# Kernel optimization log

Measured on AMD Instinct MI355X. Metric: run time of the kernel, lower is better.

Reference implementation:

```python
import jax, jax.numpy as jnp
import numpy as np

N = 100000
IN_CH, HID_CH, OUT_CH = 128, 128, 64
E = 1600000


def gcn_layer(x, W, b, src, dst, num_nodes):
    """PyG GCNConv: add self-loops, symmetric deg^-1/2 normalization,
    x' = D^-1/2 (A+I) D^-1/2 (x W) + b."""
    # degrees including self-loops (deg = 1 + in-degree with unit edge weights)
    ones = jnp.ones(dst.shape[0], dtype=x.dtype)
    deg = jnp.ones(num_nodes, dtype=x.dtype).at[dst].add(ones)
    dinv = jax.lax.rsqrt(deg)
    h = x @ W  # [N, out_dim] -- transform before propagate (PyG order)
    # neighbor messages
    norm = dinv[src] * dinv[dst]                      # [E]
    msg = h[src] * norm[:, None]                      # [E, out_dim] (traffic-bound)
    agg = jax.ops.segment_sum(msg, dst, num_segments=num_nodes)
    # self-loop contribution: norm_ii = dinv[i]^2
    agg = agg + h * (dinv * dinv)[:, None]
    return agg + b


def setup_inputs() -> dict:
    key = jax.random.key(0)
    ks = jax.random.split(key, 7)
    x = jax.random.normal(ks[0], (N, IN_CH), dtype=jnp.float32)
    edge_index = jax.random.randint(ks[1], (2, E), 0, N, dtype=jnp.int64)
    # Glorot-style init like PyG GCNConv
    W1 = jax.random.normal(ks[2], (IN_CH, HID_CH), dtype=jnp.float32) * (1.0 / np.sqrt(IN_CH))
    b1 = jnp.zeros((HID_CH,), dtype=jnp.float32)
    W2 = jax.random.normal(ks[3], (HID_CH, OUT_CH), dtype=jnp.float32) * (1.0 / np.sqrt(HID_CH))
    b2 = jnp.zeros((OUT_CH,), dtype=jnp.float32)
    return {"x": x, "edge_index": edge_index, "W1": W1, "b1": b1, "W2": W2, "b2": b2}


def reference(x, edge_index, W1, b1, W2, b2):
    src, dst = edge_index[0], edge_index[1]
    h = gcn_layer(x, W1, b1, src, dst, N)
    h = jax.nn.relu(h)  # dropout is identity in eval mode
    out = gcn_layer(h, W2, b2, src, dst, N)
    return out
```

## Files before the change

### kernel.cpp

```cpp
#include <hip/hip_runtime.h>
#include <hip/hip_fp16.h>

#define NNODES 100000
#define NEDGES 1600000
#define IN_C   128
#define HID_C  128
#define OUT_C  64

#define CAP     64
#define OVF_MAX 4096

#define BUCKET_SHIFT 7
#define BUCKET_NODES 128
#define NB ((NNODES + BUCKET_NODES - 1) / BUCKET_NODES)
#define BCAP 3072
#define BCNT_STRIDE 16
#define EB 4096
#define NBLK_A ((NEDGES + EB - 1) / EB)

typedef __attribute__((ext_vector_type(8))) _Float16 half8;
typedef __attribute__((ext_vector_type(4))) _Float16 half4;
typedef __attribute__((ext_vector_type(4))) float floatx4;

__device__ __forceinline__ long long load_idx(const void* p, long long i, int is64) {
  return is64 ? ((const long long*)p)[i] : (long long)((const int*)p)[i];
}

__global__ void detect_idx_kernel(const void* eidx, int* flag) {
  const unsigned* w = (const unsigned*)eidx;
  int lane = threadIdx.x & 63;
  unsigned v = w[2 * lane + 1];
  unsigned long long bad = __ballot(v != 0u);
  if (lane == 0) *flag = (bad == 0ull) ? 1 : 0;
}


__global__ void zero_misc_kernel(int* bcnt, int* ovf_cnt, int* ovfA_cnt) {
  int i = blockIdx.x * 256 + threadIdx.x;
  if (i < NB * BCNT_STRIDE) bcnt[i] = 0;
  if (i == 0) { *ovf_cnt = 0; *ovfA_cnt = 0; }
}

__global__ __launch_bounds__(256) void binA_kernel(const void* __restrict__ eidx,
                                                   const int* __restrict__ flag,
                                                   int* __restrict__ bcnt,
                                                   unsigned* __restrict__ buf,
                                                   int* __restrict__ ovfA_cnt,
                                                   int2* __restrict__ ovfA) {
  __shared__ unsigned se[EB];
  __shared__ unsigned short be[EB];
  __shared__ int hist[NB];
  __shared__ int base[NB];
  __shared__ int ofs[NB];
  const int tid = threadIdx.x;
  const int e0 = blockIdx.x * EB;
  const int e1 = min(e0 + EB, NEDGES);
  const int m = e1 - e0;
  const int is64 = *flag;

  for (int b = tid; b < NB; b += 256) { hist[b] = 0; ofs[b] = 0; }
  __syncthreads();

  for (int k = tid; k < m; k += 256) {
    int e = e0 + k;
    int s = (int)load_idx(eidx, e, is64);
    int d = (int)load_idx(eidx, (long long)NEDGES + e, is64);
    int b = d >> BUCKET_SHIFT;
    se[k] = (unsigned)s | ((unsigned)(d & (BUCKET_NODES - 1)) << 17);
    be[k] = (unsigned short)b;
    atomicAdd(&hist[b], 1);
  }
  __syncthreads();

  int rot = (blockIdx.x * 131) % NB;
  for (int idx = tid; idx < NB; idx += 256) {
    int b = idx + rot;
    if (b >= NB) b -= NB;
    int h = hist[b];
    if (h > 0) base[b] = atomicAdd(&bcnt[b * BCNT_STRIDE], h);
  }
  __syncthreads();

  for (int k = tid; k < m; k += 256) {
    unsigned u = se[k];
    int b = be[k];
    int ko = atomicAdd(&ofs[b], 1);
    int slot = base[b] + ko;
    if (slot < BCAP) {
      buf[(size_t)b * BCAP + slot] = u;
    } else {
      int p = atomicAdd(ovfA_cnt, 1);
      if (p < OVF_MAX)
        ovfA[p] = make_int2((int)(u & 0x1FFFFu),
                            (b << BUCKET_SHIFT) | (int)(u >> 17));
    }
  }
}

__global__ __launch_bounds__(256) void binB_kernel(const int* __restrict__ bcnt,
                                                   const unsigned* __restrict__ buf,
                                                   int* __restrict__ cnt,
                                                   float* __restrict__ dinv,
                                                   int* __restrict__ pad_csr,
                                                   int* __restrict__ ovf_cnt,
                                                   int2* __restrict__ ovf) {
  __shared__ int pad[BUCKET_NODES * CAP];
  __shared__ int lcnt[BUCKET_NODES];
  const int b = blockIdx.x;
  const int tid = threadIdx.x;
  const int node0 = b << BUCKET_SHIFT;

  if (tid < BUCKET_NODES) lcnt[tid] = 0;
  __syncthreads();

  const int n = min(bcnt[b * BCNT_STRIDE], BCAP);
  for (int k = tid; k < n; k += 256) {
    unsigned u = buf[(size_t)b * BCAP + k];
    int s = (int)(u & 0x1FFFFu);
    int dl = (int)(u >> 17);
    int slot = atomicAdd(&lcnt[dl], 1);
    if (slot < CAP) {
      pad[dl * CAP + slot] = s;
    } else {
      int p = atomicAdd(ovf_cnt, 1);
      if (p < OVF_MAX) ovf[p] = make_int2(s, node0 + dl);
    }
  }
  __syncthreads();

  constexpr int I4PN = CAP / 4;
  for (int q = tid; q < BUCKET_NODES * I4PN; q += 256) {
    int dl = q / I4PN;
    int gn = node0 + dl;
    if (gn < NNODES) {
      int c = (q % I4PN) * 4;
      *(int4*)&pad_csr[(size_t)gn * CAP + c] = *(const int4*)&pad[dl * CAP + c];
    }
  }
  if (tid < BUCKET_NODES && node0 + tid < NNODES) {
    int c = lcnt[tid];
    cnt[node0 + tid] = c;
    dinv[node0 + tid] = rsqrtf((float)(c + 1));
  }
}

__global__ void fixup_kernel(const int* __restrict__ ovfA_cnt,
                             const int2* __restrict__ ovfA,
                             int* __restrict__ cnt, float* __restrict__ dinv,
                             int* __restrict__ pad_csr,
                             int* __restrict__ ovf_cnt, int2* __restrict__ ovf) {
  int n = min(*ovfA_cnt, OVF_MAX);
  for (int t = threadIdx.x; t < n; t += 256) {
    int2 p = ovfA[t];
    int k = atomicAdd(&cnt[p.y], 1);
    if (k < CAP) {
      pad_csr[(size_t)p.y * CAP + k] = p.x;
    } else {
      int q = atomicAdd(ovf_cnt, 1);
      if (q < OVF_MAX) ovf[q] = p;
    }
  }
  __syncthreads();
  for (int t = threadIdx.x; t < n; t += 256) {
    int node = ovfA[t].y;
    dinv[node] = rsqrtf((float)(cnt[node] + 1));
  }
}

struct F8 {
  float x0, x1, x2, x3, x4, x5, x6, x7;
};

__device__ __forceinline__ void add_h8(F8& a, const __half* p) {
  int4 r = *(const int4*)p;
  const __half2* h = (const __half2*)&r;
  float2 f0 = __half22float2(h[0]);
  float2 f1 = __half22float2(h[1]);
  float2 f2 = __half22float2(h[2]);
  float2 f3 = __half22float2(h[3]);
  a.x0 += f0.x; a.x1 += f0.y; a.x2 += f1.x; a.x3 += f1.y;
  a.x4 += f2.x; a.x5 += f2.y; a.x6 += f3.x; a.x7 += f3.y;
}

template <int C, bool RELU, bool OUT16>
__global__ __launch_bounds__(256) void gather_kernel(const int* __restrict__ cnt,
                                                     const int* __restrict__ pad_csr,
                                                     const float* __restrict__ dinv,
                                                     const __half* __restrict__ Hs,
                                                     const float* __restrict__ bias,
                                                     const int* __restrict__ ovf_cnt,
                                                     const int2* __restrict__ ovf,
                                                     void* __restrict__ OutPtr) {
  constexpr int TPN = C / 16;
  int gid = blockIdx.x * 256 + threadIdx.x;
  int i = gid / TPN;
  int c16 = (gid % TPN) * 16;
  if (i >= NNODES) return;

  const float di = dinv[i];
  const int deg = cnt[i];
  const int beg = i * CAP;
  const int end = beg + min(deg, CAP);
  const int* __restrict__ lst = pad_csr;
  const __half* __restrict__ Hb = Hs + c16;

  F8 a0l = {}, a0h = {}, a1l = {}, a1h = {};
  {
    const __half* p = Hb + (size_t)i * C;
    add_h8(a0l, p);
    add_h8(a0h, p + 8);
  }

  int j = beg;
  for (; j + 8 <= end; j += 8) {
    int4 sa = *(const int4*)&lst[j];
    int4 sb = *(const int4*)&lst[j + 4];
    const __half* p0 = Hb + (size_t)sa.x * C;
    const __half* p1 = Hb + (size_t)sa.y * C;
    const __half* p2 = Hb + (size_t)sa.z * C;
    const __half* p3 = Hb + (size_t)sa.w * C;
    add_h8(a0l, p0); add_h8(a0h, p0 + 8);
    add_h8(a1l, p1); add_h8(a1h, p1 + 8);
    add_h8(a0l, p2); add_h8(a0h, p2 + 8);
    add_h8(a1l, p3); add_h8(a1h, p3 + 8);
    const __half* p4 = Hb + (size_t)sb.x * C;
    const __half* p5 = Hb + (size_t)sb.y * C;
    const __half* p6 = Hb + (size_t)sb.z * C;
    const __half* p7 = Hb + (size_t)sb.w * C;
    add_h8(a0l, p4); add_h8(a0h, p4 + 8);
    add_h8(a1l, p5); add_h8(a1h, p5 + 8);
    add_h8(a0l, p6); add_h8(a0h, p6 + 8);
    add_h8(a1l, p7); add_h8(a1h, p7 + 8);
  }
  for (; j + 2 <= end; j += 2) {
    const __half* p0 = Hb + (size_t)lst[j] * C;
    const __half* p1 = Hb + (size_t)lst[j + 1] * C;
    add_h8(a0l, p0); add_h8(a0h, p0 + 8);
    add_h8(a1l, p1); add_h8(a1h, p1 + 8);
  }
  if (j < end) {
    const __half* p0 = Hb + (size_t)lst[j] * C;
    add_h8(a0l, p0); add_h8(a0h, p0 + 8);
  }

  if (deg > CAP) {
    int n = min(*ovf_cnt, OVF_MAX);
    for (int t = 0; t < n; ++t) {
      int2 p = ovf[t];
      if (p.y == i) {
        const __half* q = Hb + (size_t)p.x * C;
        add_h8(a0l, q); add_h8(a0h, q + 8);
      }
    }
  }

  float s0 = a0l.x0 + a1l.x0, s1 = a0l.x1 + a1l.x1;
  float s2 = a0l.x2 + a1l.x2, s3 = a0l.x3 + a1l.x3;
  float s4 = a0l.x4 + a1l.x4, s5 = a0l.x5 + a1l.x5;
  float s6 = a0l.x6 + a1l.x6, s7 = a0l.x7 + a1l.x7;
  float s8 = a0h.x0 + a1h.x0, s9 = a0h.x1 + a1h.x1;
  float s10 = a0h.x2 + a1h.x2, s11 = a0h.x3 + a1h.x3;
  float s12 = a0h.x4 + a1h.x4, s13 = a0h.x5 + a1h.x5;
  float s14 = a0h.x6 + a1h.x6, s15 = a0h.x7 + a1h.x7;

  float4 b0 = *(const float4*)&bias[c16];
  float4 b1 = *(const float4*)&bias[c16 + 4];
  float4 b2 = *(const float4*)&bias[c16 + 8];
  float4 b3 = *(const float4*)&bias[c16 + 12];
  float o0 = fmaf(s0, di, b0.x),  o1 = fmaf(s1, di, b0.y);
  float o2 = fmaf(s2, di, b0.z),  o3 = fmaf(s3, di, b0.w);
  float o4 = fmaf(s4, di, b1.x),  o5 = fmaf(s5, di, b1.y);
  float o6 = fmaf(s6, di, b1.z),  o7 = fmaf(s7, di, b1.w);
  float o8 = fmaf(s8, di, b2.x),  o9 = fmaf(s9, di, b2.y);
  float o10 = fmaf(s10, di, b2.z), o11 = fmaf(s11, di, b2.w);
  float o12 = fmaf(s12, di, b3.x), o13 = fmaf(s13, di, b3.y);
  float o14 = fmaf(s14, di, b3.z), o15 = fmaf(s15, di, b3.w);
  if (RELU) {
    o0 = o0 > 0.f ? o0 : 0.f;   o1 = o1 > 0.f ? o1 : 0.f;
    o2 = o2 > 0.f ? o2 : 0.f;   o3 = o3 > 0.f ? o3 : 0.f;
    o4 = o4 > 0.f ? o4 : 0.f;   o5 = o5 > 0.f ? o5 : 0.f;
    o6 = o6 > 0.f ? o6 : 0.f;   o7 = o7 > 0.f ? o7 : 0.f;
    o8 = o8 > 0.f ? o8 : 0.f;   o9 = o9 > 0.f ? o9 : 0.f;
    o10 = o10 > 0.f ? o10 : 0.f; o11 = o11 > 0.f ? o11 : 0.f;
    o12 = o12 > 0.f ? o12 : 0.f; o13 = o13 > 0.f ? o13 : 0.f;
    o14 = o14 > 0.f ? o14 : 0.f; o15 = o15 > 0.f ? o15 : 0.f;
  }
  if (OUT16) {
    _Float16* Out = (_Float16*)OutPtr + (size_t)i * C + c16;
    half8 hv0 = {(_Float16)o0, (_Float16)o1, (_Float16)o2, (_Float16)o3,
                 (_Float16)o4, (_Float16)o5, (_Float16)o6, (_Float16)o7};
    half8 hv1 = {(_Float16)o8, (_Float16)o9, (_Float16)o10, (_Float16)o11,
                 (_Float16)o12, (_Float16)o13, (_Float16)o14, (_Float16)o15};
    *(half8*)Out = hv0;
    *(half8*)(Out + 8) = hv1;
  } else {
    float* Out = (float*)OutPtr + (size_t)i * C + c16;
    *(float4*)Out = make_float4(o0, o1, o2, o3);
    *(float4*)(Out + 4) = make_float4(o4, o5, o6, o7);
    *(float4*)(Out + 8) = make_float4(o8, o9, o10, o11);
    *(float4*)(Out + 12) = make_float4(o12, o13, o14, o15);
  }
}

template <int K, int N, bool A_F16>
__global__ __launch_bounds__(256) void mfma_gemm_kernel(const void* __restrict__ Xv,
                                                        const float* __restrict__ Wm,
                                                        const float* __restrict__ scale,
                                                        _Float16* __restrict__ Hout,
                                                        int M) {
  constexpr int KP = K + 8;
  __shared__ alignas(16) _Float16 Alds[64 * KP];
  __shared__ alignas(16) _Float16 Wlds[N * KP];

  const int tid = threadIdx.x;
  const int row0 = blockIdx.x * 64;

  constexpr int TILES = (K / 4) * (N / 4);
  for (int tile = tid; tile < TILES; tile += 256) {
    int kt = tile / (N / 4);
    int nt = tile % (N / 4);
    const float* wp = &Wm[(4 * kt) * N + 4 * nt];
    float4 r0 = *(const float4*)(wp);
    float4 r1 = *(const float4*)(wp + N);
    float4 r2 = *(const float4*)(wp + 2 * N);
    float4 r3 = *(const float4*)(wp + 3 * N);
    half4 c0 = {(_Float16)r0.x, (_Float16)r1.x, (_Float16)r2.x, (_Float16)r3.x};
    half4 c1 = {(_Float16)r0.y, (_Float16)r1.y, (_Float16)r2.y, (_Float16)r3.y};
    half4 c2 = {(_Float16)r0.z, (_Float16)r1.z, (_Float16)r2.z, (_Float16)r3.z};
    half4 c3 = {(_Float16)r0.w, (_Float16)r1.w, (_Float16)r2.w, (_Float16)r3.w};
    *(half4*)&Wlds[(4 * nt + 0) * KP + 4 * kt] = c0;
    *(half4*)&Wlds[(4 * nt + 1) * KP + 4 * kt] = c1;
    *(half4*)&Wlds[(4 * nt + 2) * KP + 4 * kt] = c2;
    *(half4*)&Wlds[(4 * nt + 3) * KP + 4 * kt] = c3;
  }

  if (A_F16) {
    const _Float16* Xh = (const _Float16*)Xv;
    constexpr int H8PR = K / 8;
    constexpr int TOT = 64 * H8PR;
    for (int idx = tid; idx < TOT; idx += 256) {
      int lr = idx / H8PR;
      int c8 = (idx % H8PR) * 8;
      int gr = row0 + lr;
      if (gr > M - 1) gr = M - 1;
      int4 v = *(const int4*)&Xh[(size_t)gr * K + c8];
      *(int4*)&Alds[lr * KP + c8] = v;
    }
  } else {
    const float* Xf = (const float*)Xv;
    constexpr int F4PR = K / 4;
    constexpr int TOT = 64 * F4PR;
    for (int idx = tid; idx < TOT; idx += 256) {
      int lr = idx / F4PR;
      int c4 = (idx % F4PR) * 4;
      int gr = row0 + lr;
      if (gr > M - 1) gr = M - 1;
      float4 v = *(const float4*)&Xf[(size_t)gr * K + c4];
      half4 h = {(_Float16)v.x, (_Float16)v.y, (_Float16)v.z, (_Float16)v.w};
      *(half4*)&Alds[lr * KP + c4] = h;
    }
  }
  __syncthreads();

  const int w = tid >> 6;
  const int lane = tid & 63;
  const int g = lane >> 4;
  const int mi = lane & 15;
  constexpr int NT = N / 16;

  floatx4 acc[NT];
#pragma unroll
  for (int t = 0; t < NT; ++t) acc[t] = (floatx4){0.f, 0.f, 0.f, 0.f};

  const _Float16* arow = &Alds[(w * 16 + mi) * KP];
#pragma unroll
  for (int ks = 0; ks < K / 32; ++ks) {
    half8 a = *(const half8*)(arow + ks * 32 + g * 8);
#pragma unroll
    for (int t = 0; t < NT; ++t) {
      half8 b = *(const half8*)&Wlds[(t * 16 + mi) * KP + ks * 32 + g * 8];
      acc[t] = __builtin_amdgcn_mfma_f32_16x16x32_f16(a, b, acc[t], 0, 0, 0);
    }
  }

#pragma unroll
  for (int r = 0; r < 4; ++r) {
    int grow = row0 + w * 16 + 4 * g + r;
    if (grow < M) {
      float s = scale[grow];
      _Float16* orow = Hout + (size_t)grow * N + mi;
#pragma unroll
      for (int t = 0; t < NT; ++t) orow[t * 16] = (_Float16)(acc[t][r] * s);
    }
  }
}

extern "C" void kernel_launch(void* const* d_in, const int* in_sizes, int n_in,
                              void* d_out, int out_size, void* d_ws, size_t ws_size,
                              hipStream_t stream) {
  const float* x = (const float*)d_in[0];
  const void* eidx = d_in[1];
  const float* W1 = (const float*)d_in[2];
  const float* b1 = (const float*)d_in[3];
  const float* W2 = (const float*)d_in[4];
  const float* b2 = (const float*)d_in[5];
  float* out = (float*)d_out;
  char* ws = (char*)d_ws;

  int*      flag     = (int*)(ws + 0);
  int*      ovf_cnt  = (int*)(ws + 512);
  int*      ovfA_cnt = (int*)(ws + 1024);
  int*      bcnt     = (int*)(ws + 1536);
  int*      cnt      = (int*)(ws + 52224);
  float*    dinv     = (float*)(ws + 452608);
  int2*     ovf      = (int2*)(ws + 852992);
  int2*     ovfA     = (int2*)(ws + 885760);
  unsigned* buf      = (unsigned*)(ws + 918528);
  int*      pad_csr  = (int*)(ws + 10528256);
  _Float16* h1       = (_Float16*)(ws + 36128256);
  _Float16* hidden   = (_Float16*)(ws + 61728256);
  _Float16* h2 = h1;

  detect_idx_kernel<<<1, 64, 0, stream>>>(eidx, flag);
  zero_misc_kernel<<<(NB * BCNT_STRIDE + 255) / 256, 256, 0, stream>>>(bcnt, ovf_cnt,
                                                                       ovfA_cnt);
  binA_kernel<<<NBLK_A, 256, 0, stream>>>(eidx, flag, bcnt, buf, ovfA_cnt, ovfA);
  binB_kernel<<<NB, 256, 0, stream>>>(bcnt, buf, cnt, dinv, pad_csr, ovf_cnt, ovf);
  fixup_kernel<<<1, 256, 0, stream>>>(ovfA_cnt, ovfA, cnt, dinv, pad_csr,
                                      ovf_cnt, ovf);

  const int GB = (NNODES + 63) / 64;
  mfma_gemm_kernel<IN_C, HID_C, false>
      <<<GB, 256, 0, stream>>>(x, W1, dinv, h1, NNODES);
  gather_kernel<HID_C, true, true>
      <<<(NNODES * (HID_C / 16) + 255) / 256, 256, 0, stream>>>(cnt, pad_csr, dinv,
                                                                (const __half*)h1, b1,
                                                                ovf_cnt, ovf, hidden);
  mfma_gemm_kernel<HID_C, OUT_C, true>
      <<<GB, 256, 0, stream>>>(hidden, W2, dinv, h2, NNODES);
  gather_kernel<OUT_C, false, false>
      <<<(NNODES * (OUT_C / 16) + 255) / 256, 256, 0, stream>>>(cnt, pad_csr, dinv,
                                                                (const __half*)h2, b2,
                                                                ovf_cnt, ovf, out);
}
```

Measured before the change: 277.0 us.

## Fuse graph binning with first GEMM and first gather with second GEMM

Merges the detect and zero kernels, runs edge binning and the layer-1 GEMM in one horizontally fused launch, and folds the overflow fixup into binB. The GEMM no longer depends on dinv, so the source-side normalization moves into the gathers, which now load dinv per neighbor. The layer-1 gather is fused with the layer-2 GEMM through shared memory, which removes the hidden-tensor round trip and several launches. The cost is extra per-edge dinv loads and a larger 512-thread block for the fused gather+GEMM.

```diff
diff --git a/kernel.cpp b/kernel.cpp
--- a/kernel.cpp
+++ b/kernel.cpp
@@ -17,6 +17,7 @@
 #define BCNT_STRIDE 16
 #define EB 4096
 #define NBLK_A ((NEDGES + EB - 1) / EB)
+#define GB ((NNODES + 63) / 64)
 
 typedef __attribute__((ext_vector_type(8))) _Float16 half8;
 typedef __attribute__((ext_vector_type(4))) _Float16 half4;
@@ -26,79 +27,147 @@
   return is64 ? ((const long long*)p)[i] : (long long)((const int*)p)[i];
 }
 
-__global__ void detect_idx_kernel(const void* eidx, int* flag) {
-  const unsigned* w = (const unsigned*)eidx;
-  int lane = threadIdx.x & 63;
-  unsigned v = w[2 * lane + 1];
-  unsigned long long bad = __ballot(v != 0u);
-  if (lane == 0) *flag = (bad == 0ull) ? 1 : 0;
-}
-
-
-__global__ void zero_misc_kernel(int* bcnt, int* ovf_cnt, int* ovfA_cnt) {
+__global__ void zero_detect_kernel(const void* eidx, int* flag, int* bcnt,
+                                   int* ovf_cnt, int* ovfA_cnt) {
   int i = blockIdx.x * 256 + threadIdx.x;
   if (i < NB * BCNT_STRIDE) bcnt[i] = 0;
   if (i == 0) { *ovf_cnt = 0; *ovfA_cnt = 0; }
-}
-
-__global__ __launch_bounds__(256) void binA_kernel(const void* __restrict__ eidx,
-                                                   const int* __restrict__ flag,
-                                                   int* __restrict__ bcnt,
-                                                   unsigned* __restrict__ buf,
-                                                   int* __restrict__ ovfA_cnt,
-                                                   int2* __restrict__ ovfA) {
-  __shared__ unsigned se[EB];
-  __shared__ unsigned short be[EB];
-  __shared__ int hist[NB];
-  __shared__ int base[NB];
-  __shared__ int ofs[NB];
+  if (blockIdx.x == 0 && threadIdx.x < 64) {
+    const unsigned* w = (const unsigned*)eidx;
+    unsigned v = w[2 * threadIdx.x + 1];
+    unsigned long long bad = __ballot(v != 0u);
+    if (threadIdx.x == 0) *flag = (bad == 0ull) ? 1 : 0;
+  }
+}
+
+__global__ __launch_bounds__(256) void binA_gemm1_kernel(
+    const void* __restrict__ eidx, const int* __restrict__ flag,
+    int* __restrict__ bcnt, unsigned* __restrict__ buf,
+    int* __restrict__ ovfA_cnt, int2* __restrict__ ovfA,
+    const float* __restrict__ x, const float* __restrict__ W1,
+    _Float16* __restrict__ h1) {
+  __shared__ alignas(16) char smem[52224];
   const int tid = threadIdx.x;
-  const int e0 = blockIdx.x * EB;
-  const int e1 = min(e0 + EB, NEDGES);
-  const int m = e1 - e0;
-  const int is64 = *flag;
-
-  for (int b = tid; b < NB; b += 256) { hist[b] = 0; ofs[b] = 0; }
-  __syncthreads();
-
-  for (int k = tid; k < m; k += 256) {
-    int e = e0 + k;
-    int s = (int)load_idx(eidx, e, is64);
-    int d = (int)load_idx(eidx, (long long)NEDGES + e, is64);
-    int b = d >> BUCKET_SHIFT;
-    se[k] = (unsigned)s | ((unsigned)(d & (BUCKET_NODES - 1)) << 17);
-    be[k] = (unsigned short)b;
-    atomicAdd(&hist[b], 1);
-  }
-  __syncthreads();
-
-  int rot = (blockIdx.x * 131) % NB;
-  for (int idx = tid; idx < NB; idx += 256) {
-    int b = idx + rot;
-    if (b >= NB) b -= NB;
-    int h = hist[b];
-    if (h > 0) base[b] = atomicAdd(&bcnt[b * BCNT_STRIDE], h);
-  }
-  __syncthreads();
-
-  for (int k = tid; k < m; k += 256) {
-    unsigned u = se[k];
-    int b = be[k];
-    int ko = atomicAdd(&ofs[b], 1);
-    int slot = base[b] + ko;
-    if (slot < BCAP) {
-      buf[(size_t)b * BCAP + slot] = u;
-    } else {
-      int p = atomicAdd(ovfA_cnt, 1);
-      if (p < OVF_MAX)
-        ovfA[p] = make_int2((int)(u & 0x1FFFFu),
-                            (b << BUCKET_SHIFT) | (int)(u >> 17));
+
+  if (blockIdx.x < NBLK_A) {
+    unsigned* se = (unsigned*)smem;
+    unsigned short* be = (unsigned short*)(smem + 16384);
+    int* hist = (int*)(smem + 24576);
+    int* base = (int*)(smem + 27712);
+    int* ofs  = (int*)(smem + 30848);
+
+    const int e0 = blockIdx.x * EB;
+    const int e1 = min(e0 + EB, NEDGES);
+    const int m = e1 - e0;
+    const int is64 = *flag;
+
+    for (int b = tid; b < NB; b += 256) { hist[b] = 0; ofs[b] = 0; }
+    __syncthreads();
+
+    for (int k = tid; k < m; k += 256) {
+      int e = e0 + k;
+      int s = (int)load_idx(eidx, e, is64);
+      int d = (int)load_idx(eidx, (long long)NEDGES + e, is64);
+      int b = d >> BUCKET_SHIFT;
+      se[k] = (unsigned)s | ((unsigned)(d & (BUCKET_NODES - 1)) << 17);
+      be[k] = (unsigned short)b;
+      atomicAdd(&hist[b], 1);
+    }
+    __syncthreads();
+
+    int rot = (blockIdx.x * 131) % NB;
+    for (int idx = tid; idx < NB; idx += 256) {
+      int b = idx + rot;
+      if (b >= NB) b -= NB;
+      int h = hist[b];
+      if (h > 0) base[b] = atomicAdd(&bcnt[b * BCNT_STRIDE], h);
+    }
+    __syncthreads();
+
+    for (int k = tid; k < m; k += 256) {
+      unsigned u = se[k];
+      int b = be[k];
+      int ko = atomicAdd(&ofs[b], 1);
+      int slot = base[b] + ko;
+      if (slot < BCAP) {
+        buf[(size_t)b * BCAP + slot] = u;
+      } else {
+        int p = atomicAdd(ovfA_cnt, 1);
+        if (p < OVF_MAX)
+          ovfA[p] = make_int2((int)(u & 0x1FFFFu),
+                              (b << BUCKET_SHIFT) | (int)(u >> 17));
+      }
+    }
+  } else {
+    constexpr int K = IN_C, N = HID_C, KP = K + 8;
+    _Float16* Alds = (_Float16*)smem;
+    _Float16* Wlds = (_Float16*)(smem + 17408);
+    const int row0 = (blockIdx.x - NBLK_A) * 64;
+
+    constexpr int TILES = (K / 4) * (N / 4);
+    for (int tile = tid; tile < TILES; tile += 256) {
+      int kt = tile / (N / 4);
+      int nt = tile % (N / 4);
+      const float* wp = &W1[(4 * kt) * N + 4 * nt];
+      float4 r0 = *(const float4*)(wp);
+      float4 r1 = *(const float4*)(wp + N);
+      float4 r2 = *(const float4*)(wp + 2 * N);
+      float4 r3 = *(const float4*)(wp + 3 * N);
+      half4 c0 = {(_Float16)r0.x, (_Float16)r1.x, (_Float16)r2.x, (_Float16)r3.x};
+      half4 c1 = {(_Float16)r0.y, (_Float16)r1.y, (_Float16)r2.y, (_Float16)r3.y};
+      half4 c2 = {(_Float16)r0.z, (_Float16)r1.z, (_Float16)r2.z, (_Float16)r3.z};
+      half4 c3 = {(_Float16)r0.w, (_Float16)r1.w, (_Float16)r2.w, (_Float16)r3.w};
+      *(half4*)&Wlds[(4 * nt + 0) * KP + 4 * kt] = c0;
+      *(half4*)&Wlds[(4 * nt + 1) * KP + 4 * kt] = c1;
+      *(half4*)&Wlds[(4 * nt + 2) * KP + 4 * kt] = c2;
+      *(half4*)&Wlds[(4 * nt + 3) * KP + 4 * kt] = c3;
+    }
+    constexpr int F4PR = K / 4;
+    for (int idx = tid; idx < 64 * F4PR; idx += 256) {
+      int lr = idx / F4PR;
+      int c4 = (idx % F4PR) * 4;
+      int gr = row0 + lr;
+      if (gr > NNODES - 1) gr = NNODES - 1;
+      float4 v = *(const float4*)&x[(size_t)gr * K + c4];
+      half4 h = {(_Float16)v.x, (_Float16)v.y, (_Float16)v.z, (_Float16)v.w};
+      *(half4*)&Alds[lr * KP + c4] = h;
+    }
+    __syncthreads();
+
+    const int w = tid >> 6;
+    const int lane = tid & 63;
+    const int g = lane >> 4;
+    const int mi = lane & 15;
+    constexpr int NT = N / 16;
+    floatx4 acc[NT];
+#pragma unroll
+    for (int t = 0; t < NT; ++t) acc[t] = (floatx4){0.f, 0.f, 0.f, 0.f};
+    const _Float16* arow = &Alds[(w * 16 + mi) * KP];
+#pragma unroll
+    for (int ks = 0; ks < K / 32; ++ks) {
+      half8 a = *(const half8*)(arow + ks * 32 + g * 8);
+#pragma unroll
+      for (int t = 0; t < NT; ++t) {
+        half8 b = *(const half8*)&Wlds[(t * 16 + mi) * KP + ks * 32 + g * 8];
+        acc[t] = __builtin_amdgcn_mfma_f32_16x16x32_f16(a, b, acc[t], 0, 0, 0);
+      }
+    }
+#pragma unroll
+    for (int r = 0; r < 4; ++r) {
+      int grow = row0 + w * 16 + 4 * g + r;
+      if (grow < NNODES) {
+        _Float16* orow = h1 + (size_t)grow * N + mi;
+#pragma unroll
+        for (int t = 0; t < NT; ++t) orow[t * 16] = (_Float16)acc[t][r];
+      }
     }
   }
 }
 
 __global__ __launch_bounds__(256) void binB_kernel(const int* __restrict__ bcnt,
                                                    const unsigned* __restrict__ buf,
+                                                   const int* __restrict__ ovfA_cnt,
+                                                   const int2* __restrict__ ovfA,
                                                    int* __restrict__ cnt,
                                                    float* __restrict__ dinv,
                                                    int* __restrict__ pad_csr,
@@ -126,6 +195,20 @@
       if (p < OVF_MAX) ovf[p] = make_int2(s, node0 + dl);
     }
   }
+  int na = min(*ovfA_cnt, OVF_MAX);
+  for (int t = tid; t < na; t += 256) {
+    int2 p = ovfA[t];
+    if ((p.y >> BUCKET_SHIFT) == b) {
+      int dl = p.y & (BUCKET_NODES - 1);
+      int slot = atomicAdd(&lcnt[dl], 1);
+      if (slot < CAP) {
+        pad[dl * CAP + slot] = p.x;
+      } else {
+        int q = atomicAdd(ovf_cnt, 1);
+        if (q < OVF_MAX) ovf[q] = make_int2(p.x, p.y);
+      }
+    }
+  }
   __syncthreads();
 
   constexpr int I4PN = CAP / 4;
@@ -144,182 +227,40 @@
   }
 }
 
-__global__ void fixup_kernel(const int* __restrict__ ovfA_cnt,
-                             const int2* __restrict__ ovfA,
-                             int* __restrict__ cnt, float* __restrict__ dinv,
-                             int* __restrict__ pad_csr,
-                             int* __restrict__ ovf_cnt, int2* __restrict__ ovf) {
-  int n = min(*ovfA_cnt, OVF_MAX);
-  for (int t = threadIdx.x; t < n; t += 256) {
-    int2 p = ovfA[t];
-    int k = atomicAdd(&cnt[p.y], 1);
-    if (k < CAP) {
-      pad_csr[(size_t)p.y * CAP + k] = p.x;
-    } else {
-      int q = atomicAdd(ovf_cnt, 1);
-      if (q < OVF_MAX) ovf[q] = p;
-    }
-  }
-  __syncthreads();
-  for (int t = threadIdx.x; t < n; t += 256) {
-    int node = ovfA[t].y;
-    dinv[node] = rsqrtf((float)(cnt[node] + 1));
-  }
-}
-
 struct F8 {
   float x0, x1, x2, x3, x4, x5, x6, x7;
 };
 
-__device__ __forceinline__ void add_h8(F8& a, const __half* p) {
+__device__ __forceinline__ void add_h8s(F8& a, const __half* p, float s) {
   int4 r = *(const int4*)p;
   const __half2* h = (const __half2*)&r;
   float2 f0 = __half22float2(h[0]);
   float2 f1 = __half22float2(h[1]);
   float2 f2 = __half22float2(h[2]);
   float2 f3 = __half22float2(h[3]);
-  a.x0 += f0.x; a.x1 += f0.y; a.x2 += f1.x; a.x3 += f1.y;
-  a.x4 += f2.x; a.x5 += f2.y; a.x6 += f3.x; a.x7 += f3.y;
-}
-
-template <int C, bool RELU, bool OUT16>
-__global__ __launch_bounds__(256) void gather_kernel(const int* __restrict__ cnt,
-                                                     const int* __restrict__ pad_csr,
-                                                     const float* __restrict__ dinv,
-                                                     const __half* __restrict__ Hs,
-                                                     const float* __restrict__ bias,
-                                                     const int* __restrict__ ovf_cnt,
-                                                     const int2* __restrict__ ovf,
-                                                     void* __restrict__ OutPtr) {
-  constexpr int TPN = C / 16;
-  int gid = blockIdx.x * 256 + threadIdx.x;
-  int i = gid / TPN;
-  int c16 = (gid % TPN) * 16;
-  if (i >= NNODES) return;
-
-  const float di = dinv[i];
-  const int deg = cnt[i];
-  const int beg = i * CAP;
-  const int end = beg + min(deg, CAP);
-  const int* __restrict__ lst = pad_csr;
-  const __half* __restrict__ Hb = Hs + c16;
-
-  F8 a0l = {}, a0h = {}, a1l = {}, a1h = {};
-  {
-    const __half* p = Hb + (size_t)i * C;
-    add_h8(a0l, p);
-    add_h8(a0h, p + 8);
-  }
-
-  int j = beg;
-  for (; j + 8 <= end; j += 8) {
-    int4 sa = *(const int4*)&lst[j];
-    int4 sb = *(const int4*)&lst[j + 4];
-    const __half* p0 = Hb + (size_t)sa.x * C;
-    const __half* p1 = Hb + (size_t)sa.y * C;
-    const __half* p2 = Hb + (size_t)sa.z * C;
-    const __half* p3 = Hb + (size_t)sa.w * C;
-    add_h8(a0l, p0); add_h8(a0h, p0 + 8);
-    add_h8(a1l, p1); add_h8(a1h, p1 + 8);
-    add_h8(a0l, p2); add_h8(a0h, p2 + 8);
-    add_h8(a1l, p3); add_h8(a1h, p3 + 8);
-    const __half* p4 = Hb + (size_t)sb.x * C;
-    const __half* p5 = Hb + (size_t)sb.y * C;
-    const __half* p6 = Hb + (size_t)sb.z * C;
-    const __half* p7 = Hb + (size_t)sb.w * C;
-    add_h8(a0l, p4); add_h8(a0h, p4 + 8);
-    add_h8(a1l, p5); add_h8(a1h, p5 + 8);
-    add_h8(a0l, p6); add_h8(a0h, p6 + 8);
-    add_h8(a1l, p7); add_h8(a1h, p7 + 8);
-  }
-  for (; j + 2 <= end; j += 2) {
-    const __half* p0 = Hb + (size_t)lst[j] * C;
-    const __half* p1 = Hb + (size_t)lst[j + 1] * C;
-    add_h8(a0l, p0); add_h8(a0h, p0 + 8);
-    add_h8(a1l, p1); add_h8(a1h, p1 + 8);
-  }
-  if (j < end) {
-    const __half* p0 = Hb + (size_t)lst[j] * C;
-    add_h8(a0l, p0); add_h8(a0h, p0 + 8);
-  }
-
-  if (deg > CAP) {
-    int n = min(*ovf_cnt, OVF_MAX);
-    for (int t = 0; t < n; ++t) {
-      int2 p = ovf[t];
-      if (p.y == i) {
-        const __half* q = Hb + (size_t)p.x * C;
-        add_h8(a0l, q); add_h8(a0h, q + 8);
-      }
-    }
-  }
-
-  float s0 = a0l.x0 + a1l.x0, s1 = a0l.x1 + a1l.x1;
-  float s2 = a0l.x2 + a1l.x2, s3 = a0l.x3 + a1l.x3;
-  float s4 = a0l.x4 + a1l.x4, s5 = a0l.x5 + a1l.x5;
-  float s6 = a0l.x6 + a1l.x6, s7 = a0l.x7 + a1l.x7;
-  float s8 = a0h.x0 + a1h.x0, s9 = a0h.x1 + a1h.x1;
-  float s10 = a0h.x2 + a1h.x2, s11 = a0h.x3 + a1h.x3;
-  float s12 = a0h.x4 + a1h.x4, s13 = a0h.x5 + a1h.x5;
-  float s14 = a0h.x6 + a1h.x6, s15 = a0h.x7 + a1h.x7;
-
-  float4 b0 = *(const float4*)&bias[c16];
-  float4 b1 = *(const float4*)&bias[c16 + 4];
-  float4 b2 = *(const float4*)&bias[c16 + 8];
-  float4 b3 = *(const float4*)&bias[c16 + 12];
-  float o0 = fmaf(s0, di, b0.x),  o1 = fmaf(s1, di, b0.y);
-  float o2 = fmaf(s2, di, b0.z),  o3 = fmaf(s3, di, b0.w);
-  float o4 = fmaf(s4, di, b1.x),  o5 = fmaf(s5, di, b1.y);
-  float o6 = fmaf(s6, di, b1.z),  o7 = fmaf(s7, di, b1.w);
-  float o8 = fmaf(s8, di, b2.x),  o9 = fmaf(s9, di, b2.y);
-  float o10 = fmaf(s10, di, b2.z), o11 = fmaf(s11, di, b2.w);
-  float o12 = fmaf(s12, di, b3.x), o13 = fmaf(s13, di, b3.y);
-  float o14 = fmaf(s14, di, b3.z), o15 = fmaf(s15, di, b3.w);
-  if (RELU) {
-    o0 = o0 > 0.f ? o0 : 0.f;   o1 = o1 > 0.f ? o1 : 0.f;
-    o2 = o2 > 0.f ? o2 : 0.f;   o3 = o3 > 0.f ? o3 : 0.f;
-    o4 = o4 > 0.f ? o4 : 0.f;   o5 = o5 > 0.f ? o5 : 0.f;
-    o6 = o6 > 0.f ? o6 : 0.f;   o7 = o7 > 0.f ? o7 : 0.f;
-    o8 = o8 > 0.f ? o8 : 0.f;   o9 = o9 > 0.f ? o9 : 0.f;
-    o10 = o10 > 0.f ? o10 : 0.f; o11 = o11 > 0.f ? o11 : 0.f;
-    o12 = o12 > 0.f ? o12 : 0.f; o13 = o13 > 0.f ? o13 : 0.f;
-    o14 = o14 > 0.f ? o14 : 0.f; o15 = o15 > 0.f ? o15 : 0.f;
-  }
-  if (OUT16) {
-    _Float16* Out = (_Float16*)OutPtr + (size_t)i * C + c16;
-    half8 hv0 = {(_Float16)o0, (_Float16)o1, (_Float16)o2, (_Float16)o3,
-                 (_Float16)o4, (_Float16)o5, (_Float16)o6, (_Float16)o7};
-    half8 hv1 = {(_Float16)o8, (_Float16)o9, (_Float16)o10, (_Float16)o11,
-                 (_Float16)o12, (_Float16)o13, (_Float16)o14, (_Float16)o15};
-    *(half8*)Out = hv0;
-    *(half8*)(Out + 8) = hv1;
-  } else {
-    float* Out = (float*)OutPtr + (size_t)i * C + c16;
-    *(float4*)Out = make_float4(o0, o1, o2, o3);
-    *(float4*)(Out + 4) = make_float4(o4, o5, o6, o7);
-    *(float4*)(Out + 8) = make_float4(o8, o9, o10, o11);
-    *(float4*)(Out + 12) = make_float4(o12, o13, o14, o15);
-  }
-}
-
-template <int K, int N, bool A_F16>
-__global__ __launch_bounds__(256) void mfma_gemm_kernel(const void* __restrict__ Xv,
-                                                        const float* __restrict__ Wm,
-                                                        const float* __restrict__ scale,
-                                                        _Float16* __restrict__ Hout,
-                                                        int M) {
-  constexpr int KP = K + 8;
-  __shared__ alignas(16) _Float16 Alds[64 * KP];
-  __shared__ alignas(16) _Float16 Wlds[N * KP];
-
+  a.x0 = fmaf(s, f0.x, a.x0); a.x1 = fmaf(s, f0.y, a.x1);
+  a.x2 = fmaf(s, f1.x, a.x2); a.x3 = fmaf(s, f1.y, a.x3);
+  a.x4 = fmaf(s, f2.x, a.x4); a.x5 = fmaf(s, f2.y, a.x5);
+  a.x6 = fmaf(s, f3.x, a.x6); a.x7 = fmaf(s, f3.y, a.x7);
+}
+
+__global__ __launch_bounds__(512) void gather1_gemm2_kernel(
+    const int* __restrict__ cnt, const int* __restrict__ pad_csr,
+    const float* __restrict__ dinv, const __half* __restrict__ h1,
+    const float* __restrict__ b1, const float* __restrict__ W2,
+    const int* __restrict__ ovf_cnt, const int2* __restrict__ ovf,
+    _Float16* __restrict__ h2) {
+  constexpr int K = HID_C, N = OUT_C, KP = K + 8;
+  __shared__ alignas(16) _Float16 Hl[64 * KP];
+  __shared__ alignas(16) _Float16 W2l[N * KP];
   const int tid = threadIdx.x;
-  const int row0 = blockIdx.x * 64;
+  const int node0 = blockIdx.x * 64;
 
   constexpr int TILES = (K / 4) * (N / 4);
-  for (int tile = tid; tile < TILES; tile += 256) {
+  for (int tile = tid; tile < TILES; tile += 512) {
     int kt = tile / (N / 4);
     int nt = tile % (N / 4);
-    const float* wp = &Wm[(4 * kt) * N + 4 * nt];
+    const float* wp = &W2[(4 * kt) * N + 4 * nt];
     float4 r0 = *(const float4*)(wp);
     float4 r1 = *(const float4*)(wp + N);
     float4 r2 = *(const float4*)(wp + 2 * N);
@@ -328,37 +269,104 @@
     half4 c1 = {(_Float16)r0.y, (_Float16)r1.y, (_Float16)r2.y, (_Float16)r3.y};
     half4 c2 = {(_Float16)r0.z, (_Float16)r1.z, (_Float16)r2.z, (_Float16)r3.z};
     half4 c3 = {(_Float16)r0.w, (_Float16)r1.w, (_Float16)r2.w, (_Float16)r3.w};
-    *(half4*)&Wlds[(4 * nt + 0) * KP + 4 * kt] = c0;
-    *(half4*)&Wlds[(4 * nt + 1) * KP + 4 * kt] = c1;
-    *(half4*)&Wlds[(4 * nt + 2) * KP + 4 * kt] = c2;
-    *(half4*)&Wlds[(4 * nt + 3) * KP + 4 * kt] = c3;
-  }
-
-  if (A_F16) {
-    const _Float16* Xh = (const _Float16*)Xv;
-    constexpr int H8PR = K / 8;
-    constexpr int TOT = 64 * H8PR;
-    for (int idx = tid; idx < TOT; idx += 256) {
-      int lr = idx / H8PR;
-      int c8 = (idx % H8PR) * 8;
-      int gr = row0 + lr;
-      if (gr > M - 1) gr = M - 1;
-      int4 v = *(const int4*)&Xh[(size_t)gr * K + c8];
-      *(int4*)&Alds[lr * KP + c8] = v;
-    }
-  } else {
-    const float* Xf = (const float*)Xv;
-    constexpr int F4PR = K / 4;
-    constexpr int TOT = 64 * F4PR;
-    for (int idx = tid; idx < TOT; idx += 256) {
-      int lr = idx / F4PR;
-      int c4 = (idx % F4PR) * 4;
-      int gr = row0 + lr;
-      if (gr > M - 1) gr = M - 1;
-      float4 v = *(const float4*)&Xf[(size_t)gr * K + c4];
-      half4 h = {(_Float16)v.x, (_Float16)v.y, (_Float16)v.z, (_Float16)v.w};
-      *(half4*)&Alds[lr * KP + c4] = h;
-    }
+    *(half4*)&W2l[(4 * nt + 0) * KP + 4 * kt] = c0;
+    *(half4*)&W2l[(4 * nt + 1) * KP + 4 * kt] = c1;
+    *(half4*)&W2l[(4 * nt + 2) * KP + 4 * kt] = c2;
+    *(half4*)&W2l[(4 * nt + 3) * KP + 4 * kt] = c3;
+  }
+
+  const int il = tid >> 3;
+  const int c16 = (tid & 7) * 16;
+  const int i = node0 + il;
+
+  float o[16];
+#pragma unroll
+  for (int q = 0; q < 16; ++q) o[q] = 0.f;
+
+  if (i < NNODES) {
+    const float di = dinv[i];
+    const int deg = cnt[i];
+    const int beg = i * CAP;
+    const int end = beg + min(deg, CAP);
+    const int* __restrict__ lst = pad_csr;
+    const __half* __restrict__ Hb = h1 + c16;
+
+    F8 a0l = {}, a0h = {}, a1l = {}, a1h = {};
+    {
+      const __half* p = Hb + (size_t)i * K;
+      add_h8s(a0l, p, di);
+      add_h8s(a0h, p + 8, di);
+    }
+    int j = beg;
+    for (; j + 8 <= end; j += 8) {
+      int4 sa = *(const int4*)&lst[j];
+      int4 sb = *(const int4*)&lst[j + 4];
+      float d0 = dinv[sa.x], d1 = dinv[sa.y], d2 = dinv[sa.z], d3 = dinv[sa.w];
+      float d4 = dinv[sb.x], d5 = dinv[sb.y], d6 = dinv[sb.z], d7 = dinv[sb.w];
+      const __half* p0 = Hb + (size_t)sa.x * K;
+      const __half* p1 = Hb + (size_t)sa.y * K;
+      const __half* p2 = Hb + (size_t)sa.z * K;
+      const __half* p3 = Hb + (size_t)sa.w * K;
+      add_h8s(a0l, p0, d0); add_h8s(a0h, p0 + 8, d0);
+      add_h8s(a1l, p1, d1); add_h8s(a1h, p1 + 8, d1);
+      add_h8s(a0l, p2, d2); add_h8s(a0h, p2 + 8, d2);
+      add_h8s(a1l, p3, d3); add_h8s(a1h, p3 + 8, d3);
+      const __half* p4 = Hb + (size_t)sb.x * K;
+      const __half* p5 = Hb + (size_t)sb.y * K;
+      const __half* p6 = Hb + (size_t)sb.z * K;
+      const __half* p7 = Hb + (size_t)sb.w * K;
+      add_h8s(a0l, p4, d4); add_h8s(a0h, p4 + 8, d4);
+      add_h8s(a1l, p5, d5); add_h8s(a1h, p5 + 8, d5);
+      add_h8s(a0l, p6, d6); add_h8s(a0h, p6 + 8, d6);
+      add_h8s(a1l, p7, d7); add_h8s(a1h, p7 + 8, d7);
+    }
+    for (; j < end; ++j) {
+      int s = lst[j];
+      float ds = dinv[s];
+      const __half* p0 = Hb + (size_t)s * K;
+      add_h8s(a0l, p0, ds); add_h8s(a0h, p0 + 8, ds);
+    }
+    if (deg > CAP) {
+      int nv = min(*ovf_cnt, OVF_MAX);
+      for (int t = 0; t < nv; ++t) {
+        int2 p = ovf[t];
+        if (p.y == i) {
+          float ds = dinv[p.x];
+          const __half* q = Hb + (size_t)p.x * K;
+          add_h8s(a0l, q, ds); add_h8s(a0h, q + 8, ds);
+        }
+      }
+    }
+    float4 bb0 = *(const float4*)&b1[c16];
+    float4 bb1 = *(const float4*)&b1[c16 + 4];
+    float4 bb2 = *(const float4*)&b1[c16 + 8];
+    float4 bb3 = *(const float4*)&b1[c16 + 12];
+    o[0] = fmaf(a0l.x0 + a1l.x0, di, bb0.x);
+    o[1] = fmaf(a0l.x1 + a1l.x1, di, bb0.y);
+    o[2] = fmaf(a0l.x2 + a1l.x2, di, bb0.z);
+    o[3] = fmaf(a0l.x3 + a1l.x3, di, bb0.w);
+    o[4] = fmaf(a0l.x4 + a1l.x4, di, bb1.x);
+    o[5] = fmaf(a0l.x5 + a1l.x5, di, bb1.y);
+    o[6] = fmaf(a0l.x6 + a1l.x6, di, bb1.z);
+    o[7] = fmaf(a0l.x7 + a1l.x7, di, bb1.w);
+    o[8] = fmaf(a0h.x0 + a1h.x0, di, bb2.x);
+    o[9] = fmaf(a0h.x1 + a1h.x1, di, bb2.y);
+    o[10] = fmaf(a0h.x2 + a1h.x2, di, bb2.z);
+    o[11] = fmaf(a0h.x3 + a1h.x3, di, bb2.w);
+    o[12] = fmaf(a0h.x4 + a1h.x4, di, bb3.x);
+    o[13] = fmaf(a0h.x5 + a1h.x5, di, bb3.y);
+    o[14] = fmaf(a0h.x6 + a1h.x6, di, bb3.z);
+    o[15] = fmaf(a0h.x7 + a1h.x7, di, bb3.w);
+#pragma unroll
+    for (int q = 0; q < 16; ++q) o[q] = o[q] > 0.f ? o[q] : 0.f;
+  }
+  {
+    half8 hv0 = {(_Float16)o[0], (_Float16)o[1], (_Float16)o[2], (_Float16)o[3],
+                 (_Float16)o[4], (_Float16)o[5], (_Float16)o[6], (_Float16)o[7]};
+    half8 hv1 = {(_Float16)o[8], (_Float16)o[9], (_Float16)o[10], (_Float16)o[11],
+                 (_Float16)o[12], (_Float16)o[13], (_Float16)o[14], (_Float16)o[15]};
+    *(half8*)&Hl[il * KP + c16] = hv0;
+    *(half8*)&Hl[il * KP + c16 + 8] = hv1;
   }
   __syncthreads();
 
@@ -366,33 +374,120 @@
   const int lane = tid & 63;
   const int g = lane >> 4;
   const int mi = lane & 15;
-  constexpr int NT = N / 16;
-
-  floatx4 acc[NT];
-#pragma unroll
-  for (int t = 0; t < NT; ++t) acc[t] = (floatx4){0.f, 0.f, 0.f, 0.f};
-
-  const _Float16* arow = &Alds[(w * 16 + mi) * KP];
+  const int wrow = (w & 3) * 16;
+  const int wcol = (w >> 2) * 32;
+
+  floatx4 acc[2];
+  acc[0] = (floatx4){0.f, 0.f, 0.f, 0.f};
+  acc[1] = (floatx4){0.f, 0.f, 0.f, 0.f};
+  const _Float16* arow = &Hl[(wrow + mi) * KP];
 #pragma unroll
   for (int ks = 0; ks < K / 32; ++ks) {
     half8 a = *(const half8*)(arow + ks * 32 + g * 8);
 #pragma unroll
-    for (int t = 0; t < NT; ++t) {
-      half8 b = *(const half8*)&Wlds[(t * 16 + mi) * KP + ks * 32 + g * 8];
+    for (int t = 0; t < 2; ++t) {
+      half8 b = *(const half8*)&W2l[(wcol + t * 16 + mi) * KP + ks * 32 + g * 8];
       acc[t] = __builtin_amdgcn_mfma_f32_16x16x32_f16(a, b, acc[t], 0, 0, 0);
     }
   }
-
 #pragma unroll
   for (int r = 0; r < 4; ++r) {
-    int grow = row0 + w * 16 + 4 * g + r;
-    if (grow < M) {
-      float s = scale[grow];
-      _Float16* orow = Hout + (size_t)grow * N + mi;
-#pragma unroll
-      for (int t = 0; t < NT; ++t) orow[t * 16] = (_Float16)(acc[t][r] * s);
-    }
-  }
+    int grow = node0 + wrow + 4 * g + r;
+    if (grow < NNODES) {
+      _Float16* orow = h2 + (size_t)grow * N + wcol + mi;
+#pragma unroll
+      for (int t = 0; t < 2; ++t) orow[t * 16] = (_Float16)acc[t][r];
+    }
+  }
+}
+
+__global__ __launch_bounds__(256) void gather2_kernel(
+    const int* __restrict__ cnt, const int* __restrict__ pad_csr,
+    const float* __restrict__ dinv, const __half* __restrict__ h2,
+    const float* __restrict__ b2, const int* __restrict__ ovf_cnt,
+    const int2* __restrict__ ovf, float* __restrict__ Out) {
+  constexpr int C = OUT_C;
+  constexpr int TPN = C / 16;
+  int gid = blockIdx.x * 256 + threadIdx.x;
+  int i = gid / TPN;
+  int c16 = (gid % TPN) * 16;
+  if (i >= NNODES) return;
+
+  const float di = dinv[i];
+  const int deg = cnt[i];
+  const int beg = i * CAP;
+  const int end = beg + min(deg, CAP);
+  const int* __restrict__ lst = pad_csr;
+  const __half* __restrict__ Hb = h2 + c16;
+
+  F8 a0l = {}, a0h = {}, a1l = {}, a1h = {};
+  {
+    const __half* p = Hb + (size_t)i * C;
+    add_h8s(a0l, p, di);
+    add_h8s(a0h, p + 8, di);
+  }
+  int j = beg;
+  for (; j + 8 <= end; j += 8) {
+    int4 sa = *(const int4*)&lst[j];
+    int4 sb = *(const int4*)&lst[j + 4];
+    float d0 = dinv[sa.x], d1 = dinv[sa.y], d2 = dinv[sa.z], d3 = dinv[sa.w];
+    float d4 = dinv[sb.x], d5 = dinv[sb.y], d6 = dinv[sb.z], d7 = dinv[sb.w];
+    const __half* p0 = Hb + (size_t)sa.x * C;
+    const __half* p1 = Hb + (size_t)sa.y * C;
+    const __half* p2 = Hb + (size_t)sa.z * C;
+    const __half* p3 = Hb + (size_t)sa.w * C;
+    add_h8s(a0l, p0, d0); add_h8s(a0h, p0 + 8, d0);
+    add_h8s(a1l, p1, d1); add_h8s(a1h, p1 + 8, d1);
+    add_h8s(a0l, p2, d2); add_h8s(a0h, p2 + 8, d2);
+    add_h8s(a1l, p3, d3); add_h8s(a1h, p3 + 8, d3);
+    const __half* p4 = Hb + (size_t)sb.x * C;
+    const __half* p5 = Hb + (size_t)sb.y * C;
+    const __half* p6 = Hb + (size_t)sb.z * C;
+    const __half* p7 = Hb + (size_t)sb.w * C;
+    add_h8s(a0l, p4, d4); add_h8s(a0h, p4 + 8, d4);
+    add_h8s(a1l, p5, d5); add_h8s(a1h, p5 + 8, d5);
+    add_h8s(a0l, p6, d6); add_h8s(a0h, p6 + 8, d6);
+    add_h8s(a1l, p7, d7); add_h8s(a1h, p7 + 8, d7);
+  }
+  for (; j < end; ++j) {
+    int s = lst[j];
+    float ds = dinv[s];
+    const __half* p0 = Hb + (size_t)s * C;
+    add_h8s(a0l, p0, ds); add_h8s(a0h, p0 + 8, ds);
+  }
+  if (deg > CAP) {
+    int nv = min(*ovf_cnt, OVF_MAX);
+    for (int t = 0; t < nv; ++t) {
+      int2 p = ovf[t];
+      if (p.y == i) {
+        float ds = dinv[p.x];
+        const __half* q = Hb + (size_t)p.x * C;
+        add_h8s(a0l, q, ds); add_h8s(a0h, q + 8, ds);
+      }
+    }
+  }
+
+  float4 bb0 = *(const float4*)&b2[c16];
+  float4 bb1 = *(const float4*)&b2[c16 + 4];
+  float4 bb2 = *(const float4*)&b2[c16 + 8];
+  float4 bb3 = *(const float4*)&b2[c16 + 12];
+  float* O = Out + (size_t)i * C + c16;
+  *(float4*)O = make_float4(fmaf(a0l.x0 + a1l.x0, di, bb0.x),
+                            fmaf(a0l.x1 + a1l.x1, di, bb0.y),
+                            fmaf(a0l.x2 + a1l.x2, di, bb0.z),
+                            fmaf(a0l.x3 + a1l.x3, di, bb0.w));
+  *(float4*)(O + 4) = make_float4(fmaf(a0l.x4 + a1l.x4, di, bb1.x),
+                                  fmaf(a0l.x5 + a1l.x5, di, bb1.y),
+                                  fmaf(a0l.x6 + a1l.x6, di, bb1.z),
+                                  fmaf(a0l.x7 + a1l.x7, di, bb1.w));
+  *(float4*)(O + 8) = make_float4(fmaf(a0h.x0 + a1h.x0, di, bb2.x),
+                                  fmaf(a0h.x1 + a1h.x1, di, bb2.y),
+                                  fmaf(a0h.x2 + a1h.x2, di, bb2.z),
+                                  fmaf(a0h.x3 + a1h.x3, di, bb2.w));
+  *(float4*)(O + 12) = make_float4(fmaf(a0h.x4 + a1h.x4, di, bb3.x),
+                                   fmaf(a0h.x5 + a1h.x5, di, bb3.y),
+                                   fmaf(a0h.x6 + a1h.x6, di, bb3.z),
+                                   fmaf(a0h.x7 + a1h.x7, di, bb3.w));
 }
 
 extern "C" void kernel_launch(void* const* d_in, const int* in_sizes, int n_in,
@@ -418,28 +513,17 @@
   unsigned* buf      = (unsigned*)(ws + 918528);
   int*      pad_csr  = (int*)(ws + 10528256);
   _Float16* h1       = (_Float16*)(ws + 36128256);
-  _Float16* hidden   = (_Float16*)(ws + 61728256);
-  _Float16* h2 = h1;
-
-  detect_idx_kernel<<<1, 64, 0, stream>>>(eidx, flag);
-  zero_misc_kernel<<<(NB * BCNT_STRIDE + 255) / 256, 256, 0, stream>>>(bcnt, ovf_cnt,
-                                                                       ovfA_cnt);
-  binA_kernel<<<NBLK_A, 256, 0, stream>>>(eidx, flag, bcnt, buf, ovfA_cnt, ovfA);
-  binB_kernel<<<NB, 256, 0, stream>>>(bcnt, buf, cnt, dinv, pad_csr, ovf_cnt, ovf);
-  fixup_kernel<<<1, 256, 0, stream>>>(ovfA_cnt, ovfA, cnt, dinv, pad_csr,
-                                      ovf_cnt, ovf);
-
-  const int GB = (NNODES + 63) / 64;
-  mfma_gemm_kernel<IN_C, HID_C, false>
-      <<<GB, 256, 0, stream>>>(x, W1, dinv, h1, NNODES);
-  gather_kernel<HID_C, true, true>
-      <<<(NNODES * (HID_C / 16) + 255) / 256, 256, 0, stream>>>(cnt, pad_csr, dinv,
-                                                                (const __half*)h1, b1,
-                                                                ovf_cnt, ovf, hidden);
-  mfma_gemm_kernel<HID_C, OUT_C, true>
-      <<<GB, 256, 0, stream>>>(hidden, W2, dinv, h2, NNODES);
-  gather_kernel<OUT_C, false, false>
-      <<<(NNODES * (OUT_C / 16) + 255) / 256, 256, 0, stream>>>(cnt, pad_csr, dinv,
-                                                                (const __half*)h2, b2,
-                                                                ovf_cnt, ovf, out);
-}
+  _Float16* h2       = (_Float16*)(ws + 61728256);
+
+  zero_detect_kernel<<<(NB * BCNT_STRIDE + 255) / 256, 256, 0, stream>>>(
+      eidx, flag, bcnt, ovf_cnt, ovfA_cnt);
+  binA_gemm1_kernel<<<NBLK_A + GB, 256, 0, stream>>>(eidx, flag, bcnt, buf,
+                                                     ovfA_cnt, ovfA, x, W1, h1);
+  binB_kernel<<<NB, 256, 0, stream>>>(bcnt, buf, ovfA_cnt, ovfA, cnt, dinv,
+                                      pad_csr, ovf_cnt, ovf);
+  gather1_gemm2_kernel<<<GB, 512, 0, stream>>>(cnt, pad_csr, dinv,
+                                               (const __half*)h1, b1, W2,
+                                               ovf_cnt, ovf, h2);
+  gather2_kernel<<<(NNODES * (OUT_C / 16) + 255) / 256, 256, 0, stream>>>(
+      cnt, pad_csr, dinv, (const __half*)h2, b2, ovf_cnt, ovf, out);
+}
```

New measurement: 277.2 us. No clear change (+0.1%).
